# Performance work log

Measured on AMD Instinct MI355X. Metric: run time of the kernel, lower is better.

## Reference

```python
import jax, jax.numpy as jnp
import numpy as np
from jax import lax

HEADS = 8
HEAD_C = 16  # attention_channels // heads = 128 // 8


def setup_inputs() -> dict:
    key = jax.random.key(0)
    ks = jax.random.split(key, 16)
    N, I, H, W = 8, 128, 36, 36
    R, C, A, O = 128, 128, 128, 128  # recurrent, common, attention, out channels
    s = lambda *sh: 0.05
    inp = {
        'x': jax.random.normal(ks[0], (N, I, H, W), jnp.float32),
        # input 1x1 conv (Accumulate of single Conv, bias init 0)
        'w_in': jax.random.normal(ks[1], (R, I), jnp.float32) * 0.05,
        'b_in': jnp.zeros((R,), jnp.float32),
        # 3x3 conv on cat([x, h]) -> common channels
        'w_conv': jax.random.normal(ks[2], (C, 2 * R, 3, 3), jnp.float32) * 0.05,
        'b_conv': jnp.zeros((C,), jnp.float32),
        # q/k/v 1x1 projections (no bias)
        'wq': jax.random.normal(ks[3], (A, C), jnp.float32) * 0.05,
        'wk': jax.random.normal(ks[4], (A, C), jnp.float32) * 0.05,
        'wv': jax.random.normal(ks[5], (A, C), jnp.float32) * 0.05,
        # gate 1x1 projections on cat([z, a]) (C + A inputs)
        'w_i': jax.random.normal(ks[6], (R, C + A), jnp.float32) * 0.05,
        'b_i': jnp.full((R,), -1.0, jnp.float32),  # init_input
        'w_f': jax.random.normal(ks[7], (R, C + A), jnp.float32) * 0.05,
        'b_f': jnp.full((R,), 1.0, jnp.float32),   # init_forget
        'w_g': jax.random.normal(ks[8], (R, C + A), jnp.float32) * 0.05,
        'b_g': jnp.zeros((R,), jnp.float32),
        'w_o': jax.random.normal(ks[9], (R, C + A), jnp.float32) * 0.05,
        'b_o': jnp.zeros((R,), jnp.float32),
        # output 1x1 conv
        'w_out': jax.random.normal(ks[10], (O, R), jnp.float32) * 0.05,
        'b_out': jnp.zeros((O,), jnp.float32),
    }
    return inp


def _conv1x1(w, x, b=None):
    y = jnp.einsum('oi,nihw->nohw', w, x)
    if b is not None:
        y = y + b[None, :, None, None]
    return y


def reference(x, w_in, b_in, w_conv, b_conv, wq, wk, wv,
              w_i, b_i, w_f, b_f, w_g, b_g, w_o, b_o, w_out, b_out):
    # first timestep: past is empty -> h = c = 0
    xt = jnp.tanh(_conv1x1(w_in, x, b_in))          # [N, R, H, W]
    h0 = jnp.zeros_like(xt)
    c0 = jnp.zeros_like(xt)
    xh = jnp.concatenate([xt, h0], axis=1)          # groups=1 -> plain concat
    z = lax.conv_general_dilated(xh, w_conv, (1, 1), 'SAME') + b_conv[None, :, None, None]
    N, C, H, W = z.shape
    HW = H * W
    q = _conv1x1(wq, z).reshape(N, HEADS, HEAD_C, HW)
    k = _conv1x1(wk, z).reshape(N, HEADS, HEAD_C, HW)
    v = _conv1x1(wv, z).reshape(N, HEADS, HEAD_C, HW)
    # spatial attention over H*W tokens per head
    w_attn = jax.nn.softmax(jnp.einsum('nhcq,nhcd->nhqd', q, k), axis=-1)  # [N,heads,HW,HW]
    a = jnp.einsum('nhcd,nhqd->nhcq', v, w_attn).reshape(N, -1, H, W)      # [N,A,H,W]
    za = jnp.concatenate([z, a], axis=1)
    i = jax.nn.sigmoid(_conv1x1(w_i, za, b_i))
    f = jax.nn.sigmoid(_conv1x1(w_f, za, b_f))
    g = jnp.tanh(_conv1x1(w_g, za, b_g))
    o = jax.nn.sigmoid(_conv1x1(w_o, za, b_o))
    c = f * c0 + i * g
    h = o * jnp.tanh(c)  # dropout p=0 -> identity
    return _conv1x1(w_out, h, b_out)
```

## Files before the change

### kernel.cpp

```cpp
#include <hip/hip_runtime.h>
#include <hip/hip_bf16.h>
#include <math.h>

typedef __hip_bfloat16 bf16;
typedef __attribute__((ext_vector_type(8))) short frag8;
typedef __attribute__((ext_vector_type(4))) float f32x4;

#define HW  1296
#define CH  128
#define TT  1327104

__device__ __forceinline__ float b2f(bf16 v) { return __bfloat162float(v); }
__device__ __forceinline__ float bits2f(unsigned short u) {
    return __uint_as_float(((unsigned)u) << 16);
}
__device__ __forceinline__ float frcp(float x) { return __builtin_amdgcn_rcpf(x); }
__device__ __forceinline__ float fsigm(float x) { return frcp(1.0f + __expf(-x)); }
__device__ __forceinline__ float ftanh(float x) {
    float xc = fminf(15.0f, fmaxf(-15.0f, x));
    float e = __expf(2.0f * xc);
    return (e - 1.0f) * frcp(e + 1.0f);
}
__device__ __forceinline__ int packrh(float a, float b) {
    unsigned ua = __float_as_uint(a) + 0x8000u;
    unsigned ub = __float_as_uint(b) + 0x8000u;
    return (int)__builtin_amdgcn_perm(ub, ua, 0x07060302);
}
__device__ __forceinline__ int2 pack4(float a, float b, float c, float d) {
    int2 r; r.x = packrh(a, b); r.y = packrh(c, d); return r;
}

__device__ __forceinline__ int detect_f32(const void* w) {
    const short4* p = (const short4*)w;
    short4 v = p[threadIdx.x & 63];
    int bad = 0;
    #pragma unroll
    for (int j = 0; j < 4; ++j) {
        float f = bits2f(((const unsigned short*)&v)[j]);
        if (!(fabsf(f) <= 100.0f)) bad = 1;
    }
    return __any(bad) ? 1 : 0;
}

__global__ __launch_bounds__(256) void k_prep(
    const void* w_in, const void* w_conv, const void* wq, const void* wk, const void* wv,
    const void* w_i, const void* w_g, const void* w_o, const void* w_out,
    const void* b_in, const void* b_conv, const void* b_i, const void* b_g,
    const void* b_o, const void* b_out,
    bf16* __restrict__ Wdst, float* __restrict__ Bdst)
{
    int idx = blockIdx.x * 256 + threadIdx.x;
    const int f = detect_f32(w_in);
    if (idx < 327680) {
        const void* src; int si;
        if (idx < 16384)       { src = w_in; si = idx; }
        else if (idx < 163840) { int j = idx - 16384; int tap = j >> 14, rem = j & 16383;
                                 int o = rem >> 7, r = rem & 127;
                                 src = w_conv; si = o * 2304 + r * 9 + tap; }
        else if (idx < 212992) { int j = idx - 163840; int o = j >> 7, i = j & 127;
                                 int ws_ = o >> 7;
                                 src = ws_ == 0 ? wq : ws_ == 1 ? wk : wv;
                                 si = (o & 127) * 128 + i; }
        else if (idx < 311296) { int j = idx - 212992; int g = j >> 15, rem = j & 32767;
                                 int o = rem >> 8, k = rem & 255;
                                 src = g == 0 ? w_i : g == 1 ? w_g : w_o; si = o * 256 + k; }
        else                   { int j = idx - 311296; int o = j >> 7, i = j & 127;
                                 src = w_out; si = o * 128 + i; }
        float v = f ? ((const float*)src)[si] : b2f(((const bf16*)src)[si]);
        Wdst[idx] = __float2bfloat16(v);
    } else if (idx < 327680 + 768) {
        int j = idx - 327680; int b = j >> 7, e = j & 127;
        const void* src = b == 0 ? b_in : b == 1 ? b_conv : b == 2 ? b_i
                        : b == 3 ? b_g : b == 4 ? b_o : b_out;
        Bdst[j] = f ? ((const float*)src)[e] : b2f(((const bf16*)src)[e]);
    }
}

__global__ __launch_bounds__(256) void k_inm(const void* __restrict__ x,
                                             const void* __restrict__ wraw,
                                             const bf16* __restrict__ Wm,
                                             const float* __restrict__ bias,
                                             bf16* __restrict__ XT) {
    __shared__ short Xl[32][132];
    const int tid = threadIdx.x, wave = tid >> 6, lane = tid & 63;
    const int quad = lane >> 4, l16 = lane & 15;
    const int n = blockIdx.x;
    const int pbase = blockIdx.y * 32;
    const int obase = blockIdx.z * 32 + (wave & 1) * 16;
    const int pstrip = (wave >> 1) * 16;
    const int f = detect_f32(wraw);

    #pragma unroll
    for (int rep = 0; rep < 4; ++rep) {
        int u = tid + rep * 256;
        int i = u >> 3;
        int p4 = (u & 7) * 4;
        int p = pbase + p4;
        short4 s = {0, 0, 0, 0};
        if (p < HW) {
            size_t gi = (size_t)n * CH * HW + (size_t)i * HW + p;
            if (f) {
                float4 fv = *(const float4*)((const float*)x + gi);
                int2 pk = pack4(fv.x, fv.y, fv.z, fv.w);
                s = *(short4*)&pk;
            } else {
                s = *(const short4*)((const bf16*)x + gi);
            }
        }
        Xl[p4 + 0][i] = s.x; Xl[p4 + 1][i] = s.y;
        Xl[p4 + 2][i] = s.z; Xl[p4 + 3][i] = s.w;
    }
    __syncthreads();

    const int pl = pstrip + l16;
    f32x4 acc = {0.f, 0.f, 0.f, 0.f};
    #pragma unroll
    for (int kc = 0; kc < 4; ++kc) {
        int k = kc * 32 + quad * 8;
        short4 b0 = *(const short4*)&Xl[pl][k];
        short4 b1 = *(const short4*)&Xl[pl][k + 4];
        frag8 bf = {b0.x, b0.y, b0.z, b0.w, b1.x, b1.y, b1.z, b1.w};
        frag8 wf = *(const frag8*)&Wm[(obase + l16) * CH + k];
        acc = __builtin_amdgcn_mfma_f32_16x16x32_bf16(wf, bf, acc, 0, 0, 0);
    }

    int p = pbase + pstrip + l16;
    if (p < HW) {
        int og = obase + quad * 4;
        int2 pk = pack4(ftanh(acc[0] + bias[og + 0]), ftanh(acc[1] + bias[og + 1]),
                        ftanh(acc[2] + bias[og + 2]), ftanh(acc[3] + bias[og + 3]));
        *(int2*)((short*)XT + ((size_t)n * HW + p) * CH + og) = pk;
    }
}

template<int MODE>
__global__ __launch_bounds__(256) void k_mm(
    const bf16* __restrict__ Act, const bf16* __restrict__ Act2,
    const bf16* __restrict__ Wm, const float* __restrict__ bias,
    bf16* __restrict__ o0, bf16* __restrict__ o1, bf16* __restrict__ o2)
{
    constexpr int NW  = (MODE == 2) ? 3 : 1;
    constexpr int KW  = (MODE == 2) ? 256 : 128;
    const int tid = threadIdx.x, wave = tid >> 6, lane = tid & 63;
    const int quad = lane >> 4, l16 = lane & 15;
    const int ostrip = wave & 1, pstrip = wave >> 1;
    const int n = blockIdx.x;
    const int obase = blockIdx.z * 32 + ostrip * 16;
    const int pbase = blockIdx.y * 64 + pstrip * 32;
    const bf16* actn = Act + (size_t)n * HW * CH;
    const bool vtile = (MODE == 1) && (obase >= 256);

    const int p1 = pbase + l16, p2 = pbase + 16 + l16;
    const bool p1ok = p1 < HW, p2ok = p2 < HW;

    frag8 zf = {0, 0, 0, 0, 0, 0, 0, 0};
    f32x4 acc[NW][2];
    #pragma unroll
    for (int g = 0; g < NW; ++g) {
        acc[g][0] = (f32x4){0.f, 0.f, 0.f, 0.f};
        acc[g][1] = (f32x4){0.f, 0.f, 0.f, 0.f};
    }

    if (MODE == 0) {
        const int h1 = p1 / 36, w1 = p1 - h1 * 36;
        const int h2 = p2 / 36, w2 = p2 - h2 * 36;
        #pragma unroll
        for (int tap = 0; tap < 9; ++tap) {
            int dy = tap / 3 - 1, dx = tap - (tap / 3) * 3 - 1;
            bool ok1 = p1ok && (unsigned)(h1 + dy) < 36u && (unsigned)(w1 + dx) < 36u;
            bool ok2 = p2ok && (unsigned)(h2 + dy) < 36u && (unsigned)(w2 + dx) < 36u;
            int sh = dy * 36 + dx;
            const bf16* a1 = actn + (size_t)(p1 + sh) * CH + quad * 8;
            const bf16* a2 = actn + (size_t)(p2 + sh) * CH + quad * 8;
            const bf16* wp = Wm + tap * 16384 + (obase + l16) * CH + quad * 8;
            #pragma unroll
            for (int kc = 0; kc < 4; ++kc) {
                frag8 bf1 = zf, bf2 = zf;
                if (ok1) bf1 = *(const frag8*)&a1[kc * 32];
                if (ok2) bf2 = *(const frag8*)&a2[kc * 32];
                frag8 wf = *(const frag8*)&wp[kc * 32];
                acc[0][0] = __builtin_amdgcn_mfma_f32_16x16x32_bf16(wf, bf1, acc[0][0], 0, 0, 0);
                acc[0][1] = __builtin_amdgcn_mfma_f32_16x16x32_bf16(wf, bf2, acc[0][1], 0, 0, 0);
            }
        }
    } else {
        const bf16* act2n = (MODE == 2) ? Act2 + (size_t)n * HW * CH : nullptr;
        #pragma unroll
        for (int kc = 0; kc < KW / 32; ++kc) {
            const bf16* src = (MODE == 2 && kc >= 4) ? act2n : actn;
            int ko = (MODE == 2 ? (kc & 3) : kc) * 32 + quad * 8;
            frag8 bf1 = zf, bf2 = zf;
            if (p1ok) bf1 = *(const frag8*)&src[(size_t)p1 * CH + ko];
            if (p2ok) bf2 = *(const frag8*)&src[(size_t)p2 * CH + ko];
            #pragma unroll
            for (int g = 0; g < NW; ++g) {
                const bf16* wp = Wm + g * 32768 + (obase + l16) * KW + kc * 32 + quad * 8;
                frag8 wf = *(const frag8*)wp;
                if (vtile) {
                    acc[g][0] = __builtin_amdgcn_mfma_f32_16x16x32_bf16(bf1, wf, acc[g][0], 0, 0, 0);
                    acc[g][1] = __builtin_amdgcn_mfma_f32_16x16x32_bf16(bf2, wf, acc[g][1], 0, 0, 0);
                } else {
                    acc[g][0] = __builtin_amdgcn_mfma_f32_16x16x32_bf16(wf, bf1, acc[g][0], 0, 0, 0);
                    acc[g][1] = __builtin_amdgcn_mfma_f32_16x16x32_bf16(wf, bf2, acc[g][1], 0, 0, 0);
                }
            }
        }
    }

    if (vtile) {
        int ov = (obase - 256) + l16;
        #pragma unroll
        for (int pt = 0; pt < 2; ++pt) {
            int p4 = pbase + pt * 16 + quad * 4;
            if (p4 >= HW) continue;
            int2 pk = pack4(acc[0][pt][0], acc[0][pt][1], acc[0][pt][2], acc[0][pt][3]);
            *(int2*)((short*)o2 + ((size_t)n * CH + ov) * HW + p4) = pk;
        }
        return;
    }
    const int og = obase + quad * 4;
    #pragma unroll
    for (int pt = 0; pt < 2; ++pt) {
        int p = pbase + pt * 16 + l16;
        if (p >= HW) continue;
        size_t rowoff = ((size_t)n * HW + p) * CH;
        if (MODE == 0) {
            int2 pk = pack4(acc[0][pt][0] + bias[og + 0], acc[0][pt][1] + bias[og + 1],
                            acc[0][pt][2] + bias[og + 2], acc[0][pt][3] + bias[og + 3]);
            *(int2*)((short*)o0 + rowoff + og) = pk;
        } else if (MODE == 1) {
            int which = og >> 7, ol = og & 127;
            bf16* dst = which == 0 ? o0 : o1;
            size_t di = (((size_t)n * 8 + (ol >> 4)) * HW + p) * 16 + (ol & 15);
            int2 pk = pack4(acc[0][pt][0], acc[0][pt][1], acc[0][pt][2], acc[0][pt][3]);
            *(int2*)((short*)dst + di) = pk;
        } else {
            float hv[4];
            #pragma unroll
            for (int r = 0; r < 4; ++r) {
                int o = og + r;
                float iv = fsigm(acc[0][pt][r] + bias[o]);
                float gv = ftanh(acc[1][pt][r] + bias[128 + o]);
                float ov = fsigm(acc[2][pt][r] + bias[256 + o]);
                hv[r] = ov * ftanh(iv * gv);
            }
            int2 pk = pack4(hv[0], hv[1], hv[2], hv[3]);
            *(int2*)((short*)o0 + rowoff + og) = pk;
        }
    }
}

__global__ __launch_bounds__(256) void k_outm(const bf16* __restrict__ Hb,
                                              const bf16* __restrict__ Wm,
                                              const float* __restrict__ bias,
                                              void* __restrict__ out,
                                              const void* __restrict__ wraw) {
    const int tid = threadIdx.x, wave = tid >> 6, lane = tid & 63;
    const int quad = lane >> 4, l16 = lane & 15;
    const int pstrip = wave & 1, ostrip = wave >> 1;
    const int n = blockIdx.x;
    const int pbase = blockIdx.y * 32 + pstrip * 16;
    const int obase = blockIdx.z * 64 + ostrip * 32;
    if (pbase >= HW) return;
    const int f32f = detect_f32(wraw);
    const bf16* hn = Hb + (size_t)n * HW * CH;
    const int pa = pbase + l16;

    f32x4 acc0 = {0.f, 0.f, 0.f, 0.f}, acc1 = {0.f, 0.f, 0.f, 0.f};
    #pragma unroll
    for (int kc = 0; kc < 4; ++kc) {
        int ko = kc * 32 + quad * 8;
        frag8 af = *(const frag8*)&hn[(size_t)pa * CH + ko];
        frag8 b0 = *(const frag8*)&Wm[(obase + l16) * CH + ko];
        frag8 b1 = *(const frag8*)&Wm[(obase + 16 + l16) * CH + ko];
        acc0 = __builtin_amdgcn_mfma_f32_16x16x32_bf16(af, b0, acc0, 0, 0, 0);
        acc1 = __builtin_amdgcn_mfma_f32_16x16x32_bf16(af, b1, acc1, 0, 0, 0);
    }
    int p4 = pbase + quad * 4;
    #pragma unroll
    for (int ot = 0; ot < 2; ++ot) {
        int o = obase + ot * 16 + l16;
        f32x4 a = ot ? acc1 : acc0;
        float bv = bias[o];
        size_t di = ((size_t)n * CH + o) * HW + p4;
        if (f32f) {
            float4 fv = {a[0] + bv, a[1] + bv, a[2] + bv, a[3] + bv};
            *(float4*)&((float*)out)[di] = fv;
        } else {
            int2 pk = pack4(a[0] + bv, a[1] + bv, a[2] + bv, a[3] + bv);
            *(int2*)&((short*)out)[di] = pk;
        }
    }
}

__global__ __launch_bounds__(1024) void k_attn(const bf16* __restrict__ Qg,
                                               const bf16* __restrict__ Kg,
                                               const bf16* __restrict__ Vcf,
                                               bf16* __restrict__ A) {
    __shared__ __align__(16) short Pl[16][16][72];
    __shared__ float Ocomb[3][4][16][17];
    __shared__ float Lcomb[3][4][16];

    const int tid = threadIdx.x;
    const int w = tid >> 6, lane = tid & 63;
    const int quad = lane >> 4, l16 = lane & 15;
    const int qw = w & 3, dq = w >> 2;
    const int n = blockIdx.x;
    const int qb = blockIdx.y * 64;
    const int head = blockIdx.z;
    const short* Qh = (const short*)Qg + ((size_t)(n * 8 + head)) * HW * 16;
    const short* Kh = (const short*)Kg + ((size_t)(n * 8 + head)) * HW * 16;
    const short* Vh = (const short*)Vcf + ((size_t)n * CH + head * 16) * HW;

    frag8 zf = {0, 0, 0, 0, 0, 0, 0, 0};
    frag8 qf = zf;
    const int qtok = qb + qw * 16 + l16;
    if (quad < 2 && qtok < HW)
        qf = *(const frag8*)&Qh[(size_t)qtok * 16 + quad * 8];

    f32x4 Oacc = {0.f, 0.f, 0.f, 0.f};
    float lsum = 0.0f;
    short* plrow = &Pl[w][l16][0];

    const int cstart = dq ? (1 + 5 * dq) : 0;
    const int cend   = 6 + 5 * dq;
    for (int ci = cstart; ci < cend; ++ci) {
        int d0 = ci * 64;
        bool last = (ci == 20);
        f32x4 ST[4];
        #pragma unroll
        for (int t = 0; t < 4; ++t) {
            frag8 kf = zf;
            if (quad < 2)
                kf = *(const frag8*)&Kh[(size_t)(d0 + t * 16 + l16) * 16 + quad * 8];
            f32x4 zacc = {0.f, 0.f, 0.f, 0.f};
            ST[t] = __builtin_amdgcn_mfma_f32_16x16x32_bf16(kf, qf, zacc, 0, 0, 0);
        }
        #pragma unroll
        for (int t = 0; t < 4; ++t) {
            float pf0 = __expf(ST[t][0]);
            float pf1 = __expf(ST[t][1]);
            float pf2 = __expf(ST[t][2]);
            float pf3 = __expf(ST[t][3]);
            if (last) {
                int dg = d0 + t * 16 + quad * 4;
                if (dg + 0 >= HW) pf0 = 0.0f;
                if (dg + 1 >= HW) pf1 = 0.0f;
                if (dg + 2 >= HW) pf2 = 0.0f;
                if (dg + 3 >= HW) pf3 = 0.0f;
            }
            lsum += (pf0 + pf1) + (pf2 + pf3);
            *(int2*)&plrow[t * 16 + quad * 4] = pack4(pf0, pf1, pf2, pf3);
        }
        #pragma unroll
        for (int s = 0; s < 2; ++s) {
            frag8 vf = *(const frag8*)&Vh[(size_t)l16 * HW + d0 + s * 32 + quad * 8];
            frag8 pf = *(const frag8*)&plrow[s * 32 + quad * 8];
            Oacc = __builtin_amdgcn_mfma_f32_16x16x32_bf16(vf, pf, Oacc, 0, 0, 0);
        }
    }

    lsum += __shfl_xor(lsum, 16);
    lsum += __shfl_xor(lsum, 32);

    if (dq > 0) {
        int slot = dq - 1;
        #pragma unroll
        for (int r = 0; r < 4; ++r)
            Ocomb[slot][qw][quad * 4 + r][l16] = Oacc[r];
        if (quad == 0) Lcomb[slot][qw][l16] = lsum;
    }
    __syncthreads();
    if (dq == 0) {
        #pragma unroll
        for (int s = 0; s < 3; ++s) {
            #pragma unroll
            for (int r = 0; r < 4; ++r)
                Oacc[r] += Ocomb[s][qw][quad * 4 + r][l16];
            lsum += Lcomb[s][qw][l16];
        }
        if (qtok < HW) {
            float inv = frcp(lsum);
            int2 pk = pack4(Oacc[0] * inv, Oacc[1] * inv, Oacc[2] * inv, Oacc[3] * inv);
            short* An = (short*)A + (size_t)n * HW * CH;
            *(int2*)&An[(size_t)qtok * CH + head * 16 + quad * 4] = pk;
        }
    }
}

extern "C" void kernel_launch(void* const* d_in, const int* in_sizes, int n_in,
                              void* d_out, int out_size, void* d_ws, size_t ws_size,
                              hipStream_t stream) {
    char* ws = (char*)d_ws;
    bf16*  Wst  = (bf16*)(ws + 256);
    float* Bst  = (float*)(ws + 655616);
    bf16*  XT   = (bf16*)(ws + 1048576);
    bf16*  Zb   = XT + TT;
    bf16*  Qb   = Zb + TT;
    bf16*  Kb   = Qb + TT;
    bf16*  Vb   = Kb + TT;
    bf16*  Ab   = Vb + TT;
    bf16*  Hb   = Ab + TT;

    k_prep<<<1284, 256, 0, stream>>>(d_in[1], d_in[3], d_in[5], d_in[6], d_in[7],
                                     d_in[8], d_in[12], d_in[14], d_in[16],
                                     d_in[2], d_in[4], d_in[9], d_in[13], d_in[15], d_in[17],
                                     Wst, Bst);
    k_inm<<<dim3(8, 41, 4), 256, 0, stream>>>(d_in[0], d_in[1], Wst, Bst, XT);
    k_mm<0><<<dim3(8, 21, 4), 256, 0, stream>>>(XT, nullptr, Wst + 16384, Bst + 128,
                                                Zb, nullptr, nullptr);
    k_mm<1><<<dim3(8, 21, 12), 256, 0, stream>>>(Zb, nullptr, Wst + 163840, nullptr,
                                                 Qb, Kb, Vb);
    k_attn<<<dim3(8, 21, 8), 1024, 0, stream>>>(Qb, Kb, Vb, Ab);
    k_mm<2><<<dim3(8, 21, 4), 256, 0, stream>>>(Zb, Ab, Wst + 212992, Bst + 256,
                                                Hb, nullptr, nullptr);
    k_outm<<<dim3(8, 41, 2), 256, 0, stream>>>(Hb, Wst + 311296, Bst + 640, d_out, d_in[1]);
}
```

Before: 212.0 us.

## Rewrite attention with 32x32 MFMA, register-resident probabilities and MFMA row sums

Rewrites the attention kernel so each wave handles 32 queries using 32x32x16 bf16 MFMA. Probabilities stay in registers and are rearranged with permlane32_swap rather than staged through LDS. The softmax denominator comes from a ones row folded into the V operand, and exp2 is used with the Q weights prescaled by log2(e) in prep. Cross-wave partial-sum combining and block-level synchronisation are removed, and K/V fragments are software-prefetched, in exchange for more registers per wave and the loss of split-key parallelism within a block.

Result: faster. 200.9 us (-5.3%).

```diff
diff --git a/kernel.cpp b/kernel.cpp
--- a/kernel.cpp
+++ b/kernel.cpp
@@ -5,6 +5,9 @@
 typedef __hip_bfloat16 bf16;
 typedef __attribute__((ext_vector_type(8))) short frag8;
 typedef __attribute__((ext_vector_type(4))) float f32x4;
+typedef __attribute__((ext_vector_type(16))) float f32x16;
+typedef __attribute__((ext_vector_type(2))) unsigned int u32x2;
+typedef __attribute__((ext_vector_type(4))) unsigned int u32x4;
 
 #define HW  1296
 #define CH  128
@@ -28,6 +31,11 @@
 }
 __device__ __forceinline__ int2 pack4(float a, float b, float c, float d) {
     int2 r; r.x = packrh(a, b); r.y = packrh(c, d); return r;
+}
+__device__ __forceinline__ unsigned cvtpk(float a, float b) {
+    unsigned r;
+    asm("v_cvt_pk_bf16_f32 %0, %1, %2" : "=v"(r) : "v"(a), "v"(b));
+    return r;
 }
 
 __device__ __forceinline__ int detect_f32(const void* w) {
@@ -67,6 +75,7 @@
         else                   { int j = idx - 311296; int o = j >> 7, i = j & 127;
                                  src = w_out; si = o * 128 + i; }
         float v = f ? ((const float*)src)[si] : b2f(((const bf16*)src)[si]);
+        if (idx >= 163840 && idx < 180224) v *= 1.4426950408889634f;
         Wdst[idx] = __float2bfloat16(v);
     } else if (idx < 327680 + 768) {
         int j = idx - 327680; int b = j >> 7, e = j & 127;
@@ -293,98 +302,99 @@
     }
 }
 
-__global__ __launch_bounds__(1024) void k_attn(const bf16* __restrict__ Qg,
-                                               const bf16* __restrict__ Kg,
-                                               const bf16* __restrict__ Vcf,
-                                               bf16* __restrict__ A) {
-    __shared__ __align__(16) short Pl[16][16][72];
-    __shared__ float Ocomb[3][4][16][17];
-    __shared__ float Lcomb[3][4][16];
-
+__global__ __launch_bounds__(256) void k_attn(const bf16* __restrict__ Qg,
+                                              const bf16* __restrict__ Kg,
+                                              const bf16* __restrict__ Vcf,
+                                              bf16* __restrict__ A) {
     const int tid = threadIdx.x;
     const int w = tid >> 6, lane = tid & 63;
-    const int quad = lane >> 4, l16 = lane & 15;
-    const int qw = w & 3, dq = w >> 2;
+    const int l32 = lane & 31, hi = lane >> 5;
     const int n = blockIdx.x;
-    const int qb = blockIdx.y * 64;
     const int head = blockIdx.z;
+    const int qb = blockIdx.y * 128 + w * 32;
+    if (qb >= HW) return;
+    const int qtok = qb + l32;
+
     const short* Qh = (const short*)Qg + ((size_t)(n * 8 + head)) * HW * 16;
     const short* Kh = (const short*)Kg + ((size_t)(n * 8 + head)) * HW * 16;
     const short* Vh = (const short*)Vcf + ((size_t)n * CH + head * 16) * HW;
 
-    frag8 zf = {0, 0, 0, 0, 0, 0, 0, 0};
-    frag8 qf = zf;
-    const int qtok = qb + qw * 16 + l16;
-    if (quad < 2 && qtok < HW)
-        qf = *(const frag8*)&Qh[(size_t)qtok * 16 + quad * 8];
-
-    f32x4 Oacc = {0.f, 0.f, 0.f, 0.f};
-    float lsum = 0.0f;
-    short* plrow = &Pl[w][l16][0];
-
-    const int cstart = dq ? (1 + 5 * dq) : 0;
-    const int cend   = 6 + 5 * dq;
-    for (int ci = cstart; ci < cend; ++ci) {
-        int d0 = ci * 64;
-        bool last = (ci == 20);
-        f32x4 ST[4];
-        #pragma unroll
-        for (int t = 0; t < 4; ++t) {
-            frag8 kf = zf;
-            if (quad < 2)
-                kf = *(const frag8*)&Kh[(size_t)(d0 + t * 16 + l16) * 16 + quad * 8];
-            f32x4 zacc = {0.f, 0.f, 0.f, 0.f};
-            ST[t] = __builtin_amdgcn_mfma_f32_16x16x32_bf16(kf, qf, zacc, 0, 0, 0);
-        }
-        #pragma unroll
-        for (int t = 0; t < 4; ++t) {
-            float pf0 = __expf(ST[t][0]);
-            float pf1 = __expf(ST[t][1]);
-            float pf2 = __expf(ST[t][2]);
-            float pf3 = __expf(ST[t][3]);
-            if (last) {
-                int dg = d0 + t * 16 + quad * 4;
-                if (dg + 0 >= HW) pf0 = 0.0f;
-                if (dg + 1 >= HW) pf1 = 0.0f;
-                if (dg + 2 >= HW) pf2 = 0.0f;
-                if (dg + 3 >= HW) pf3 = 0.0f;
-            }
-            lsum += (pf0 + pf1) + (pf2 + pf3);
-            *(int2*)&plrow[t * 16 + quad * 4] = pack4(pf0, pf1, pf2, pf3);
-        }
-        #pragma unroll
-        for (int s = 0; s < 2; ++s) {
-            frag8 vf = *(const frag8*)&Vh[(size_t)l16 * HW + d0 + s * 32 + quad * 8];
-            frag8 pf = *(const frag8*)&plrow[s * 32 + quad * 8];
-            Oacc = __builtin_amdgcn_mfma_f32_16x16x32_bf16(vf, pf, Oacc, 0, 0, 0);
-        }
-    }
-
-    lsum += __shfl_xor(lsum, 16);
-    lsum += __shfl_xor(lsum, 32);
-
-    if (dq > 0) {
-        int slot = dq - 1;
-        #pragma unroll
-        for (int r = 0; r < 4; ++r)
-            Ocomb[slot][qw][quad * 4 + r][l16] = Oacc[r];
-        if (quad == 0) Lcomb[slot][qw][l16] = lsum;
-    }
-    __syncthreads();
-    if (dq == 0) {
-        #pragma unroll
-        for (int s = 0; s < 3; ++s) {
-            #pragma unroll
-            for (int r = 0; r < 4; ++r)
-                Oacc[r] += Ocomb[s][qw][quad * 4 + r][l16];
-            lsum += Lcomb[s][qw][l16];
-        }
-        if (qtok < HW) {
-            float inv = frcp(lsum);
-            int2 pk = pack4(Oacc[0] * inv, Oacc[1] * inv, Oacc[2] * inv, Oacc[3] * inv);
-            short* An = (short*)A + (size_t)n * HW * CH;
-            *(int2*)&An[(size_t)qtok * CH + head * 16 + quad * 4] = pk;
-        }
+    frag8 qf = {0, 0, 0, 0, 0, 0, 0, 0};
+    if (qtok < HW) qf = *(const frag8*)&Qh[(size_t)qtok * 16 + hi * 8];
+
+    const short one = (short)0x3F80;
+    const frag8 vones = {one, one, one, one, one, one, one, one};
+    const frag8 vzero = {0, 0, 0, 0, 0, 0, 0, 0};
+    const frag8 vfill = (l32 == 16) ? vones : vzero;
+    const bool vload = l32 < 16;
+    const short* Vrow = Vh + (size_t)(vload ? l32 : 0) * HW;
+
+    const f32x16 zero16 = {};
+    f32x16 Oacc = {};
+
+    auto KLD = [&](int dd) -> frag8 {
+        return *(const frag8*)&Kh[(size_t)(dd + l32) * 16 + hi * 8];
+    };
+    auto VLD = [&](int dd) -> frag8 {
+        return vload ? *(const frag8*)&Vrow[dd + hi * 8] : vfill;
+    };
+
+    frag8 kf = KLD(0);
+    frag8 va = VLD(0), vb = VLD(16);
+
+    for (int it = 0; it < 40; ++it) {
+        const int d0 = it * 32;
+        f32x16 S = __builtin_amdgcn_mfma_f32_32x32x16_bf16(kf, qf, zero16, 0, 0, 0);
+        frag8 kn = KLD(d0 + 32);
+        frag8 van = VLD(d0 + 32);
+        frag8 vbn = VLD(d0 + 48);
+
+        float p[16];
+        #pragma unroll
+        for (int r = 0; r < 16; ++r) p[r] = __builtin_amdgcn_exp2f(S[r]);
+
+        #pragma unroll
+        for (int hh = 0; hh < 2; ++hh) {
+            unsigned P0 = cvtpk(p[hh * 8 + 0], p[hh * 8 + 1]);
+            unsigned P1 = cvtpk(p[hh * 8 + 2], p[hh * 8 + 3]);
+            unsigned P2 = cvtpk(p[hh * 8 + 4], p[hh * 8 + 5]);
+            unsigned P3 = cvtpk(p[hh * 8 + 6], p[hh * 8 + 7]);
+            u32x2 s02 = __builtin_amdgcn_permlane32_swap(P0, P2, false, false);
+            u32x2 s13 = __builtin_amdgcn_permlane32_swap(P1, P3, false, false);
+            u32x4 bw = {s02[0], s13[0], s02[1], s13[1]};
+            frag8 pf = __builtin_bit_cast(frag8, bw);
+            Oacc = __builtin_amdgcn_mfma_f32_32x32x16_bf16(hh ? vb : va, pf, Oacc, 0, 0, 0);
+        }
+        kf = kn; va = van; vb = vbn;
+    }
+
+    {
+        f32x16 S = __builtin_amdgcn_mfma_f32_32x32x16_bf16(kf, qf, zero16, 0, 0, 0);
+        float p[8];
+        #pragma unroll
+        for (int r = 0; r < 8; ++r) p[r] = __builtin_amdgcn_exp2f(S[r]);
+        unsigned P0 = cvtpk(p[0], p[1]);
+        unsigned P1 = cvtpk(p[2], p[3]);
+        unsigned P2 = cvtpk(p[4], p[5]);
+        unsigned P3 = cvtpk(p[6], p[7]);
+        u32x2 s02 = __builtin_amdgcn_permlane32_swap(P0, P2, false, false);
+        u32x2 s13 = __builtin_amdgcn_permlane32_swap(P1, P3, false, false);
+        u32x4 bw = {s02[0], s13[0], s02[1], s13[1]};
+        frag8 pf = __builtin_bit_cast(frag8, bw);
+        Oacc = __builtin_amdgcn_mfma_f32_32x32x16_bf16(va, pf, Oacc, 0, 0, 0);
+    }
+
+    float lsum = Oacc[8];
+    u32x2 lb = __builtin_amdgcn_permlane32_swap(__float_as_uint(lsum),
+                                                __float_as_uint(lsum), false, false);
+    float inv = frcp(__uint_as_float(lb[0]));
+
+    if (qtok < HW) {
+        short* An = (short*)A + ((size_t)n * HW + qtok) * CH + head * 16;
+        int2 pk0 = pack4(Oacc[0] * inv, Oacc[1] * inv, Oacc[2] * inv, Oacc[3] * inv);
+        int2 pk1 = pack4(Oacc[4] * inv, Oacc[5] * inv, Oacc[6] * inv, Oacc[7] * inv);
+        *(int2*)&An[hi * 4] = pk0;
+        *(int2*)&An[8 + hi * 4] = pk1;
     }
 }
 
@@ -411,7 +421,7 @@
                                                 Zb, nullptr, nullptr);
     k_mm<1><<<dim3(8, 21, 12), 256, 0, stream>>>(Zb, nullptr, Wst + 163840, nullptr,
                                                  Qb, Kb, Vb);
-    k_attn<<<dim3(8, 21, 8), 1024, 0, stream>>>(Qb, Kb, Vb, Ab);
+    k_attn<<<dim3(8, 11, 8), 256, 0, stream>>>(Qb, Kb, Vb, Ab);
     k_mm<2><<<dim3(8, 21, 4), 256, 0, stream>>>(Zb, Ab, Wst + 212992, Bst + 256,
                                                 Hb, nullptr, nullptr);
     k_outm<<<dim3(8, 41, 2), 256, 0, stream>>>(Hb, Wst + 311296, Bst + 640, d_out, d_in[1]);
```
